# Kernel tuning notes

Measured on AMD Instinct MI355X. Metric: run time of the kernel, lower is better.

The kernel has to match this reference:

```python
import jax, jax.numpy as jnp
import numpy as np

R = 8
INPUT_DIM = 2048
OUTPUT_DIM = 2048
SCALING = 16.0 / R  # lora_alpha / r
TEMPERATURE = 1.0
LN_EPS = 1e-5


def setup_inputs() -> dict:
    key = jax.random.key(0)
    ks = jax.random.split(key, 6)
    bs, seq, ctr_out, ctr_final = 8, 2048, 32, 4
    x = jax.random.normal(ks[0], (bs, seq, INPUT_DIM), dtype=jnp.float32)
    ctr = jax.random.normal(ks[1], (bs, ctr_out), dtype=jnp.float32)
    W1 = jax.random.normal(ks[2], (60, ctr_out), dtype=jnp.float32) * (1.0 / np.sqrt(ctr_out))
    b1 = jnp.zeros((60,), jnp.float32)
    W2 = jax.random.normal(ks[3], (ctr_final, 60), dtype=jnp.float32) * (1.0 / np.sqrt(60))
    b2 = jnp.zeros((ctr_final,), jnp.float32)
    Wa = jax.random.normal(ks[4], (INPUT_DIM * R, ctr_final), dtype=jnp.float32) * 0.02
    Wb = jax.random.normal(ks[5], (R * OUTPUT_DIM, ctr_final), dtype=jnp.float32) * 0.02
    return {
        'x': x, 'ctr_hidden_states': ctr,
        'ln_gamma': jnp.ones((ctr_out,), jnp.float32),
        'ln_beta': jnp.zeros((ctr_out,), jnp.float32),
        'W1': W1, 'b1': b1, 'W2': W2, 'b2': b2, 'Wa': Wa, 'Wb': Wb,
    }


def reference(x, ctr_hidden_states, ln_gamma, ln_beta, W1, b1, W2, b2, Wa, Wb):
    bs = x.shape[0]
    # gating MLP (default which_in_gate branch): LN -> Linear -> ReLU -> Linear
    mu = jnp.mean(ctr_hidden_states, axis=-1, keepdims=True)
    var = jnp.mean(jnp.square(ctr_hidden_states - mu), axis=-1, keepdims=True)
    z = (ctr_hidden_states - mu) * jax.lax.rsqrt(var + LN_EPS) * ln_gamma + ln_beta
    h = jax.nn.relu(z @ W1.T + b1)                 # [bs, 60]
    gate = h @ W2.T + b2                           # [bs, ctr_final_dim]
    # soft routing with softmax
    gate = jax.nn.softmax(gate / TEMPERATURE, axis=-1)
    # per-sample low-rank adapters
    A = (gate @ Wa.T).reshape(bs, R, INPUT_DIM)    # [bs, r, d_in]
    B = (gate @ Wb.T).reshape(bs, R, OUTPUT_DIM)   # [bs, r, d_out]
    # out = (x @ A^T) @ B * scaling
    xa = jnp.einsum('bsd,brd->bsr', x, A)          # [bs, seq, r]
    out = jnp.einsum('bsr,bro->bso', xa, B) * SCALING
    return out
```

## Files before the change

kernel.cpp:

```cpp
#include <hip/hip_runtime.h>
#include <hip/hip_bf16.h>
#include <math.h>


#define BS 8
#define SEQ 2048
#define DIM 2048
#define RR 8
#define SCALING 2.0f

__global__ void gate_ab_kernel(const float* __restrict__ ctr,
                               const float* __restrict__ gamma,
                               const float* __restrict__ beta,
                               const float* __restrict__ W1,
                               const float* __restrict__ b1,
                               const float* __restrict__ W2,
                               const float* __restrict__ b2,
                               const float* __restrict__ Wa,
                               const float* __restrict__ Wb,
                               float* __restrict__ A,
                               float* __restrict__ B) {
    __shared__ float z_s[BS][32];
    __shared__ float h_s[BS][60];
    __shared__ float logit_s[BS][4];
    __shared__ float gate_s[BS][4];
    const int tid = threadIdx.x;

    {
        const int b = tid >> 5, i = tid & 31;
        float v = ctr[b * 32 + i];
        float s = v;
        #pragma unroll
        for (int m = 16; m; m >>= 1) s += __shfl_xor(s, m, 64);
        const float mu = s * (1.0f / 32.0f);
        const float d = v - mu;
        float sq = d * d;
        #pragma unroll
        for (int m = 16; m; m >>= 1) sq += __shfl_xor(sq, m, 64);
        const float var = sq * (1.0f / 32.0f);
        z_s[b][i] = d * rsqrtf(var + 1e-5f) * gamma[i] + beta[i];
    }
    __syncthreads();

    for (int idx = tid; idx < BS * 60; idx += 256) {
        const int b = idx / 60, j = idx % 60;
        float acc = b1[j];
        #pragma unroll
        for (int k = 0; k < 32; ++k) acc += z_s[b][k] * W1[j * 32 + k];
        h_s[b][j] = fmaxf(acc, 0.0f);
    }
    __syncthreads();

    if (tid < 32) {
        const int b = tid >> 2, c = tid & 3;
        float acc = b2[c];
        for (int k = 0; k < 60; ++k) acc += h_s[b][k] * W2[c * 60 + k];
        logit_s[b][c] = acc;
    }
    __syncthreads();

    if (tid < 8) {
        float m = logit_s[tid][0];
        #pragma unroll
        for (int c = 1; c < 4; ++c) m = fmaxf(m, logit_s[tid][c]);
        float e[4], s = 0.0f;
        #pragma unroll
        for (int c = 0; c < 4; ++c) { e[c] = expf(logit_s[tid][c] - m); s += e[c]; }
        const float inv = 1.0f / s;
        #pragma unroll
        for (int c = 0; c < 4; ++c) gate_s[tid][c] = e[c] * inv;
    }
    __syncthreads();

    const float4* __restrict__ Wa4 = (const float4*)Wa;
    const float4* __restrict__ Wb4 = (const float4*)Wb;
    const int total = BS * RR * DIM;
    for (int idx = blockIdx.x * 256 + tid; idx < total; idx += gridDim.x * 256) {
        const int b = idx >> 14, rd = idx & 16383;
        const float4 g = *(const float4*)gate_s[b];
        const float4 wa = Wa4[rd];
        A[idx] = g.x * wa.x + g.y * wa.y + g.z * wa.z + g.w * wa.w;
        const float4 wb = Wb4[rd];
        B[idx] = SCALING * (g.x * wb.x + g.y * wb.y + g.z * wb.z + g.w * wb.w);
    }
}

__global__ void __launch_bounds__(512, 4)
fused_kernel(const float* __restrict__ x, const float* __restrict__ A,
             const float* __restrict__ B, float* __restrict__ out) {
    __shared__ float Ts[RR * DIM];
    const int b = blockIdx.x >> 6;
    const int tile = blockIdx.x & 63;
    const int wave = threadIdx.x >> 6, lane = threadIdx.x & 63;

    {
        const float4* __restrict__ src = (const float4*)(A + b * (RR * DIM));
        float4* dst = (float4*)Ts;
        for (int i = threadIdx.x; i < RR * DIM / 4; i += 512) dst[i] = src[i];
    }
    __syncthreads();

    const float* __restrict__ xr =
        x + ((size_t)b * SEQ + tile * 32 + wave * 4) * DIM;

    float acc[4][8];
    #pragma unroll
    for (int i = 0; i < 4; ++i)
        #pragma unroll
        for (int r = 0; r < 8; ++r) acc[i][r] = 0.0f;

    float4 xcur[4], xnxt[4];
    {
        const int d0 = lane * 4;
        #pragma unroll
        for (int i = 0; i < 4; ++i)
            xcur[i] = *(const float4*)&xr[(size_t)i * DIM + d0];
    }
    #pragma unroll
    for (int j = 0; j < 8; ++j) {
        const int d = j * 256 + lane * 4;
        if (j < 7) {
            #pragma unroll
            for (int i = 0; i < 4; ++i)
                xnxt[i] = *(const float4*)&xr[(size_t)i * DIM + d + 256];
        }
        float4 a4[8];
        #pragma unroll
        for (int r = 0; r < 8; ++r) a4[r] = *(const float4*)&Ts[r * DIM + d];
        #pragma unroll
        for (int i = 0; i < 4; ++i) {
            #pragma unroll
            for (int r = 0; r < 8; ++r)
                acc[i][r] += xcur[i].x * a4[r].x + xcur[i].y * a4[r].y +
                             xcur[i].z * a4[r].z + xcur[i].w * a4[r].w;
        }
        #pragma unroll
        for (int i = 0; i < 4; ++i) xcur[i] = xnxt[i];
    }

    float xa[4][8];
    #pragma unroll
    for (int i = 0; i < 4; ++i) {
        #pragma unroll
        for (int r = 0; r < 8; ++r) {
            float v = acc[i][r];
            #pragma unroll
            for (int off = 32; off; off >>= 1) v += __shfl_xor(v, off, 64);
            xa[i][r] = v;
        }
    }

    __syncthreads();
    {
        const float4* __restrict__ src = (const float4*)(B + b * (RR * DIM));
        float4* dst = (float4*)Ts;
        for (int i = threadIdx.x; i < RR * DIM / 4; i += 512) dst[i] = src[i];
    }
    __syncthreads();

    float* __restrict__ ob =
        out + ((size_t)b * SEQ + tile * 32 + wave * 4) * DIM;
    #pragma unroll
    for (int j = 0; j < 8; ++j) {
        const int o = j * 256 + lane * 4;
        float4 b4[8];
        #pragma unroll
        for (int r = 0; r < 8; ++r) b4[r] = *(const float4*)&Ts[r * DIM + o];
        #pragma unroll
        for (int i = 0; i < 4; ++i) {
            float4 v = {0.0f, 0.0f, 0.0f, 0.0f};
            #pragma unroll
            for (int r = 0; r < 8; ++r) {
                v.x += xa[i][r] * b4[r].x;
                v.y += xa[i][r] * b4[r].y;
                v.z += xa[i][r] * b4[r].z;
                v.w += xa[i][r] * b4[r].w;
            }
            *(float4*)&ob[(size_t)i * DIM + o] = v;
        }
    }
}

extern "C" void kernel_launch(void* const* d_in, const int* in_sizes, int n_in,
                              void* d_out, int out_size, void* d_ws, size_t ws_size,
                              hipStream_t stream) {
    const float* x     = (const float*)d_in[0];
    const float* ctr   = (const float*)d_in[1];
    const float* gamma = (const float*)d_in[2];
    const float* beta  = (const float*)d_in[3];
    const float* W1    = (const float*)d_in[4];
    const float* b1    = (const float*)d_in[5];
    const float* W2    = (const float*)d_in[6];
    const float* b2    = (const float*)d_in[7];
    const float* Wa    = (const float*)d_in[8];
    const float* Wb    = (const float*)d_in[9];

    float* ws = (float*)d_ws;
    float* A  = ws;
    float* B  = ws + 131072;
    float* out = (float*)d_out;

    gate_ab_kernel<<<128, 256, 0, stream>>>(ctr, gamma, beta, W1, b1, W2, b2,
                                            Wa, Wb, A, B);
    fused_kernel<<<BS * 64, 512, 0, stream>>>(x, A, B, out);
}
```

Before: 260.4 us.

## Drop LDS staging of adapters, read A/B from cache, shrink blocks, nontemporal stores

The fused kernel no longer copies the per-sample A and B matrices into shared memory. Each wave now reads them directly from global memory, relying on L2/L1 caching. Blocks shrink to 256 threads covering 16 rows, which doubles the grid, and output writes use nontemporal stores to avoid polluting the cache. This removes the 64KB LDS footprint and its barriers, which should improve occupancy, at the cost of more global/cache traffic for A/B reads.

```diff
diff --git a/kernel.cpp b/kernel.cpp
--- a/kernel.cpp
+++ b/kernel.cpp
@@ -1,5 +1,4 @@
 #include <hip/hip_runtime.h>
-#include <hip/hip_bf16.h>
 #include <math.h>
 
 
@@ -8,6 +7,8 @@
 #define DIM 2048
 #define RR 8
 #define SCALING 2.0f
+
+typedef float vf4 __attribute__((ext_vector_type(4)));
 
 __global__ void gate_ab_kernel(const float* __restrict__ ctr,
                                const float* __restrict__ gamma,
@@ -72,36 +73,29 @@
     }
     __syncthreads();
 
-    const float4* __restrict__ Wa4 = (const float4*)Wa;
-    const float4* __restrict__ Wb4 = (const float4*)Wb;
+    const vf4* __restrict__ Wa4 = (const vf4*)Wa;
+    const vf4* __restrict__ Wb4 = (const vf4*)Wb;
     const int total = BS * RR * DIM;
     for (int idx = blockIdx.x * 256 + tid; idx < total; idx += gridDim.x * 256) {
         const int b = idx >> 14, rd = idx & 16383;
-        const float4 g = *(const float4*)gate_s[b];
-        const float4 wa = Wa4[rd];
+        const vf4 g = *(const vf4*)gate_s[b];
+        const vf4 wa = Wa4[rd];
         A[idx] = g.x * wa.x + g.y * wa.y + g.z * wa.z + g.w * wa.w;
-        const float4 wb = Wb4[rd];
+        const vf4 wb = Wb4[rd];
         B[idx] = SCALING * (g.x * wb.x + g.y * wb.y + g.z * wb.z + g.w * wb.w);
     }
 }
 
-__global__ void __launch_bounds__(512, 4)
+__global__ void __launch_bounds__(256, 4)
 fused_kernel(const float* __restrict__ x, const float* __restrict__ A,
              const float* __restrict__ B, float* __restrict__ out) {
-    __shared__ float Ts[RR * DIM];
-    const int b = blockIdx.x >> 6;
-    const int tile = blockIdx.x & 63;
+    const int b    = blockIdx.x >> 7;
+    const int tile = blockIdx.x & 127;
     const int wave = threadIdx.x >> 6, lane = threadIdx.x & 63;
 
-    {
-        const float4* __restrict__ src = (const float4*)(A + b * (RR * DIM));
-        float4* dst = (float4*)Ts;
-        for (int i = threadIdx.x; i < RR * DIM / 4; i += 512) dst[i] = src[i];
-    }
-    __syncthreads();
-
     const float* __restrict__ xr =
-        x + ((size_t)b * SEQ + tile * 32 + wave * 4) * DIM;
+        x + ((size_t)(b * SEQ + tile * 16 + wave * 4)) * DIM;
+    const float* __restrict__ Ab = A + b * (RR * DIM);
 
     float acc[4][8];
     #pragma unroll
@@ -109,12 +103,12 @@
         #pragma unroll
         for (int r = 0; r < 8; ++r) acc[i][r] = 0.0f;
 
-    float4 xcur[4], xnxt[4];
+    vf4 xcur[4], xnxt[4];
     {
         const int d0 = lane * 4;
         #pragma unroll
         for (int i = 0; i < 4; ++i)
-            xcur[i] = *(const float4*)&xr[(size_t)i * DIM + d0];
+            xcur[i] = *(const vf4*)&xr[(size_t)i * DIM + d0];
     }
     #pragma unroll
     for (int j = 0; j < 8; ++j) {
@@ -122,11 +116,11 @@
         if (j < 7) {
             #pragma unroll
             for (int i = 0; i < 4; ++i)
-                xnxt[i] = *(const float4*)&xr[(size_t)i * DIM + d + 256];
+                xnxt[i] = *(const vf4*)&xr[(size_t)i * DIM + d + 256];
         }
-        float4 a4[8];
+        vf4 a4[8];
         #pragma unroll
-        for (int r = 0; r < 8; ++r) a4[r] = *(const float4*)&Ts[r * DIM + d];
+        for (int r = 0; r < 8; ++r) a4[r] = *(const vf4*)&Ab[r * DIM + d];
         #pragma unroll
         for (int i = 0; i < 4; ++i) {
             #pragma unroll
@@ -150,25 +144,18 @@
         }
     }
 
-    __syncthreads();
-    {
-        const float4* __restrict__ src = (const float4*)(B + b * (RR * DIM));
-        float4* dst = (float4*)Ts;
-        for (int i = threadIdx.x; i < RR * DIM / 4; i += 512) dst[i] = src[i];
-    }
-    __syncthreads();
-
+    const float* __restrict__ Bb = B + b * (RR * DIM);
     float* __restrict__ ob =
-        out + ((size_t)b * SEQ + tile * 32 + wave * 4) * DIM;
+        out + ((size_t)(b * SEQ + tile * 16 + wave * 4)) * DIM;
     #pragma unroll
     for (int j = 0; j < 8; ++j) {
         const int o = j * 256 + lane * 4;
-        float4 b4[8];
+        vf4 b4[8];
         #pragma unroll
-        for (int r = 0; r < 8; ++r) b4[r] = *(const float4*)&Ts[r * DIM + o];
+        for (int r = 0; r < 8; ++r) b4[r] = *(const vf4*)&Bb[r * DIM + o];
         #pragma unroll
         for (int i = 0; i < 4; ++i) {
-            float4 v = {0.0f, 0.0f, 0.0f, 0.0f};
+            vf4 v = {0.0f, 0.0f, 0.0f, 0.0f};
             #pragma unroll
             for (int r = 0; r < 8; ++r) {
                 v.x += xa[i][r] * b4[r].x;
@@ -176,7 +163,7 @@
                 v.z += xa[i][r] * b4[r].z;
                 v.w += xa[i][r] * b4[r].w;
             }
-            *(float4*)&ob[(size_t)i * DIM + o] = v;
+            __builtin_nontemporal_store(v, (vf4*)&ob[(size_t)i * DIM + o]);
         }
     }
 }
@@ -202,5 +189,5 @@
 
     gate_ab_kernel<<<128, 256, 0, stream>>>(ctr, gamma, beta, W1, b1, W2, b2,
                                             Wa, Wb, A, B);
-    fused_kernel<<<BS * 64, 512, 0, stream>>>(x, A, B, out);
+    fused_kernel<<<BS * SEQ / 16, 256, 0, stream>>>(x, A, B, out);
 }
```

After: 463.7 us. 1.78x slower.
